# Kernel tuning notes

Hardware: AMD Instinct MI355X
Metric: run time of the kernel (lower is better)

The kernel has to match this reference:

```python
import jax, jax.numpy as jnp
import numpy as np
from jax import lax

B, V, ENC = 64, 2048, 128   # batch, total_voxels, encoder_dim
T = 100                      # max caption length
EMB, DEC, ATT, VOCAB = 256, 512, 256, 29


def setup_inputs() -> dict:
    key = jax.random.key(0)
    ks = jax.random.split(key, 24)
    u = lambda k, shape, s=0.1: jax.random.uniform(k, shape, jnp.float32, -s, s)
    inp = {}
    inp['encoder_output'] = jax.random.normal(ks[0], (B, V, ENC), jnp.float32)
    inp['captions'] = jax.random.randint(ks[1], (B, T), 0, VOCAB)
    # lengths sorted descending (torch loop assumes this); max length == T
    lens = jnp.sort(jax.random.randint(ks[2], (B,), 1, T + 1))[::-1]
    inp['caption_lengths'] = lens.at[0].set(T)
    # parameters (torch Linear: y = x @ W.T + b; kaiming-ish uniform)
    inp['emb_W'] = u(ks[3], (VOCAB, EMB))                       # embed init uniform(-0.1,0.1)
    inp['W_enc'] = u(ks[4], (ATT, ENC), ENC ** -0.5)
    inp['b_enc'] = u(ks[5], (ATT,), ENC ** -0.5)
    inp['W_dec'] = u(ks[6], (ATT, DEC), DEC ** -0.5)
    inp['b_dec'] = u(ks[7], (ATT,), DEC ** -0.5)
    inp['w_full'] = u(ks[8], (ATT,), ATT ** -0.5)               # full_att weight [1,ATT] -> vector
    inp['b_full'] = u(ks[9], (), ATT ** -0.5)
    lstm_in = EMB + ENC
    inp['W_ih'] = u(ks[10], (4 * DEC, lstm_in), DEC ** -0.5)
    inp['b_ih'] = u(ks[11], (4 * DEC,), DEC ** -0.5)
    inp['W_hh'] = u(ks[12], (4 * DEC, DEC), DEC ** -0.5)
    inp['b_hh'] = u(ks[13], (4 * DEC,), DEC ** -0.5)
    inp['W_init_h'] = u(ks[14], (DEC, ENC), ENC ** -0.5)
    inp['b_init_h'] = u(ks[15], (DEC,), ENC ** -0.5)
    inp['W_init_c'] = u(ks[16], (DEC, ENC), ENC ** -0.5)
    inp['b_init_c'] = u(ks[17], (DEC,), ENC ** -0.5)
    inp['W_beta'] = u(ks[18], (ENC, DEC), DEC ** -0.5)
    inp['b_beta'] = u(ks[19], (ENC,), DEC ** -0.5)
    inp['W_final'] = u(ks[20], (VOCAB, DEC))                    # uniform(-0.1,0.1) per init_weights
    inp['b_final'] = jnp.zeros((VOCAB,), jnp.float32)
    return inp


def reference(encoder_output, captions, caption_lengths, emb_W,
              W_enc, b_enc, W_dec, b_dec, w_full, b_full,
              W_ih, b_ih, W_hh, b_hh,
              W_init_h, b_init_h, W_init_c, b_init_c,
              W_beta, b_beta, W_final, b_final):
    # dropout in eval mode (identity) for deterministic reference
    emb = emb_W[captions]                                  # [B,T,EMB]
    enc_att = encoder_output @ W_enc.T + b_enc             # [B,V,ATT] (loop-invariant)
    mean_enc = encoder_output.mean(axis=1)                 # [B,ENC]
    h0 = mean_enc @ W_init_h.T + b_init_h                  # [B,DEC]
    c0 = mean_enc @ W_init_c.T + b_init_c
    lengths = caption_lengths

    def step(carry, xs):
        h, c = carry
        emb_t, t = xs                                      # [B,EMB], scalar
        # additive attention
        dec_att = h @ W_dec.T + b_dec                      # [B,ATT]
        scores = jax.nn.relu(enc_att + dec_att[:, None, :]) @ w_full + b_full  # [B,V]
        alpha = jax.nn.softmax(scores, axis=1)
        awe = jnp.einsum('bv,bve->be', alpha, encoder_output)                   # [B,ENC]
        gate = jax.nn.sigmoid(h @ W_beta.T + b_beta)
        awe = gate * awe
        # LSTMCell (torch gate order: i, f, g, o)
        x = jnp.concatenate([emb_t, awe], axis=1)          # [B,EMB+ENC]
        gates = x @ W_ih.T + b_ih + h @ W_hh.T + b_hh      # [B,4*DEC]
        i, f, g, o = jnp.split(gates, 4, axis=1)
        i, f, o = jax.nn.sigmoid(i), jax.nn.sigmoid(f), jax.nn.sigmoid(o)
        g = jnp.tanh(g)
        c_new = f * c + i * g
        h_new = o * jnp.tanh(c_new)
        pred = h_new @ W_final.T + b_final                 # [B,VOCAB]
        # length-based truncation: only rows with t < length are updated
        m = (t < lengths)[:, None]
        h2 = jnp.where(m, h_new, h)
        c2 = jnp.where(m, c_new, c)
        pred = jnp.where(m, pred, 0.0)
        alpha = jnp.where(m, alpha, 0.0)
        return (h2, c2), (pred, alpha)

    (_, _), (preds, alphas) = lax.scan(
        step, (h0, c0), (emb.transpose(1, 0, 2), jnp.arange(T)))
    predictions = preds.transpose(1, 0, 2)                 # [B,T,VOCAB]
    alphas = alphas.transpose(1, 0, 2)                     # [B,T,V]
    return predictions, alphas, caption_lengths
```

## Files before the change

kernel.cpp:

```cpp
#include <hip/hip_runtime.h>
#include <hip/hip_bf16.h>

#define BB 64
#define VV 2048
#define ENCD 128
#define TT 100
#define EMBD 256
#define DECD 512
#define ATTD 256
#define NVOCAB 29

typedef unsigned int u32;
typedef unsigned short u16;
typedef __attribute__((ext_vector_type(2))) float f2;

__device__ __forceinline__ float sigf(float x) { return 1.0f / (1.0f + __expf(-x)); }
__device__ __forceinline__ u16 to_bf16(float f) {
    u32 u = __float_as_uint(f);
    u += 0x7fffu + ((u >> 16) & 1u);
    return (u16)(u >> 16);
}

#if __has_builtin(__builtin_amdgcn_cvt_pk_fp8_f32) && __has_builtin(__builtin_amdgcn_cvt_pk_f32_fp8)
#define HAVE_FP8_CVT 1
#endif

__device__ __forceinline__ u32 fp8_enc(float f) {
#ifdef HAVE_FP8_CVT
    return (u32)__builtin_amdgcn_cvt_pk_fp8_f32(f, f, 0, false) & 0xffu;
#else
    u32 u = __float_as_uint(f);
    u32 s = (u >> 24) & 0x80u;
    u32 a = u & 0x7fffffffu;
    u32 r = a + 0x7FFFFu + ((a >> 20) & 1u);
    int v = (int)(r >> 20) - (120 << 3);
    if (v < 8) v = 0;
    if (v > 0x7E) v = 0x7E;
    return s | (u32)v;
#endif
}
__device__ __forceinline__ void fp8x4_dec(u32 u, float* o) {
#ifdef HAVE_FP8_CVT
    f2 lo = __builtin_amdgcn_cvt_pk_f32_fp8((int)u, false);
    f2 hi = __builtin_amdgcn_cvt_pk_f32_fp8((int)u, true);
    o[0] = lo[0]; o[1] = lo[1]; o[2] = hi[0]; o[3] = hi[1];
#else
    #pragma unroll
    for (int i = 0; i < 4; i++) {
        u32 byte = (u >> (8 * i)) & 0xffu;
        u32 s = (byte & 0x80u) << 24;
        u32 m = byte & 0x7fu;
        o[i] = m ? __uint_as_float(s | ((m + (120u << 3)) << 20)) : __uint_as_float(s);
    }
#endif
}


__global__ __launch_bounds__(256) void k_transpose(const float* __restrict__ W_dec,
                                                   const float* __restrict__ W_beta,
                                                   const float* __restrict__ W_ih,
                                                   const float* __restrict__ W_enc,
                                                   float* __restrict__ W_decT,
                                                   float* __restrict__ W_betaT,
                                                   float* __restrict__ W2T,
                                                   float* __restrict__ W_encT) {
    int i = blockIdx.x * 256 + threadIdx.x;
    if (i < DECD * ATTD) {
        int l = i / ATTD, a = i % ATTD;
        W_decT[i] = W_dec[a * DECD + l];
    } else if (i < DECD * ATTD + DECD * ENCD) {
        int j = i - DECD * ATTD;
        int l = j / ENCD, e = j % ENCD;
        W_betaT[j] = W_beta[e * DECD + l];
    } else if (i < DECD * ATTD + DECD * ENCD + ENCD * 2048) {
        int j = i - (DECD * ATTD + DECD * ENCD);
        int e = j >> 11, g = j & 2047;
        W2T[j] = W_ih[g * 384 + 256 + e];
    } else if (i < DECD * ATTD + DECD * ENCD + ENCD * 2048 + ENCD * ATTD) {
        int j = i - (DECD * ATTD + DECD * ENCD + ENCD * 2048);
        int k = j / ATTD, a = j % ATTD;
        W_encT[j] = W_enc[a * ENCD + k];
    }
}

__global__ __launch_bounds__(256) void k_mean(const float* __restrict__ enc,
                                              float* __restrict__ mpart) {
    int b = blockIdx.x >> 3, chunk = blockIdx.x & 7;
    int t = threadIdx.x;
    int e = t & 127, h = t >> 7;
    __shared__ float red[256];
    const float* src = enc + ((size_t)b * VV + chunk * 256 + h * 128) * ENCD + e;
    float s = 0.f;
    #pragma unroll 16
    for (int v = 0; v < 128; v++) s += src[(size_t)v * ENCD];
    red[t] = s;
    __syncthreads();
    if (t < 128) mpart[((size_t)b * 8 + chunk) * ENCD + t] = red[t] + red[t + 128];
}

__global__ __launch_bounds__(256) void k_enc_att(const float* __restrict__ enc,
                                                 const float* __restrict__ W_encT,
                                                 const float* __restrict__ b_enc,
                                                 unsigned char* __restrict__ enc_att8,
                                                 u16* __restrict__ enc_bf) {
    __shared__ float tile[64][ENCD + 1];
    int b = blockIdx.y, v0 = blockIdx.x * 64;
    int t = threadIdx.x;
    const float* src = enc + ((size_t)b * VV + v0) * ENCD;
    u16* dstb = enc_bf + ((size_t)b * VV + v0) * ENCD;
    for (int i = t; i < 64 * ENCD; i += 256) {
        float x = src[i];
        tile[i >> 7][i & 127] = x;
        dstb[i] = to_bf16(x);
    }
    __syncthreads();
    int vl = t & 63;
    int ag = __builtin_amdgcn_readfirstlane(t >> 6);
    int qq = v0 >> 9, vin = (v0 & 511) + vl;
    unsigned char* dst8 = enc_att8 + (((size_t)(b * 4 + qq) * 256) << 9) + vin;
    for (int ao = 0; ao < 8; ao++) {
        int a0 = ag * 64 + ao * 8;
        float acc[8];
        #pragma unroll
        for (int j = 0; j < 8; j++) acc[j] = b_enc[a0 + j];
        const float* wT = W_encT + a0;
        #pragma unroll 8
        for (int k = 0; k < ENCD; k++) {
            float x = tile[vl][k];
            #pragma unroll
            for (int j = 0; j < 8; j++) acc[j] = fmaf(x, wT[k * ATTD + j], acc[j]);
        }
        #pragma unroll
        for (int j = 0; j < 8; j++)
            dst8[(size_t)(a0 + j) << 9] = (unsigned char)fp8_enc(acc[j]);
    }
}

__global__ __launch_bounds__(512) void k_init(const float* __restrict__ mpart,
                                              const int* __restrict__ lens,
                                              const int* __restrict__ captions,
                                              const float* __restrict__ emb_W,
                                              const float* __restrict__ W_init_h,
                                              const float* __restrict__ b_init_h,
                                              const float* __restrict__ W_init_c,
                                              const float* __restrict__ b_init_c,
                                              const float* __restrict__ W_decT,
                                              const float* __restrict__ b_dec,
                                              const float* __restrict__ W_betaT,
                                              const float* __restrict__ b_beta,
                                              float* __restrict__ c0,
                                              float* __restrict__ xT,
                                              float* __restrict__ dec_att,
                                              float* __restrict__ gate0,
                                              float* __restrict__ out_len) {
    __shared__ float mean[ENCD];
    __shared__ float h_s[DECD];
    int b = blockIdx.x, t = threadIdx.x;
    if (t < ENCD) {
        const float* mp = mpart + (size_t)b * 8 * ENCD + t;
        float s = mp[0];
        #pragma unroll
        for (int i = 1; i < 8; i++) s += mp[(size_t)i * ENCD];
        mean[t] = s * (1.0f / VV);
    }
    __syncthreads();
    {
        int d = t;
        float hh = b_init_h[d], cc = b_init_c[d];
        for (int k = 0; k < ENCD; k++) {
            hh = fmaf(mean[k], W_init_h[d * ENCD + k], hh);
            cc = fmaf(mean[k], W_init_c[d * ENCD + k], cc);
        }
        c0[b * DECD + d] = cc;
        h_s[d] = hh;
        xT[(384 + d) * BB + b] = hh;
    }
    __syncthreads();
    if (t < ATTD) {
        float s2 = b_dec[t];
        for (int l = 0; l < DECD; l++) s2 = fmaf(h_s[l], W_decT[l * ATTD + t], s2);
        dec_att[b * ATTD + t] = s2;
    } else if (t < ATTD + ENCD) {
        int ee = t - ATTD;
        float s2 = b_beta[ee];
        for (int l = 0; l < DECD; l++) s2 = fmaf(h_s[l], W_betaT[l * ENCD + ee], s2);
        gate0[b * ENCD + ee] = sigf(s2);
    } else {
        int k = t - 384;
        int cap = captions[b * TT + 0];
        xT[k * BB + b] = emb_W[cap * EMBD + k];
        xT[(k + 128) * BB + b] = emb_W[cap * EMBD + k + 128];
    }
    if (t == 0) out_len[b] = (float)lens[b];
}


__global__ __launch_bounds__(256) void k_att(const unsigned char* __restrict__ enc_att8,
                                             const u16* __restrict__ enc_bf,
                                             const float* __restrict__ dec_att,
                                             const float* __restrict__ w_full,
                                             const int* __restrict__ lens,
                                             const float* __restrict__ xT,
                                             const float* __restrict__ W_ih,
                                             const float* __restrict__ W_hh,
                                             const float* __restrict__ b_ih,
                                             const float* __restrict__ b_hh,
                                             u16* __restrict__ escoreT,
                                             float* __restrict__ dpartT,
                                             float* __restrict__ pawe,
                                             float* __restrict__ gates_part, int ts) {
    int blk = blockIdx.x, t = threadIdx.x;
    int lane = t & 63, wv = t >> 6;
    if (blk < 256) {
        int b = blk >> 2, qq = blk & 3;
        if (ts >= lens[b]) return;
        __shared__ float sp[4][512];
        __shared__ float esh[512];
        __shared__ float dred[4];
        __shared__ float redw[4][ENCD];
        {
            const uint2* sp2 = (const uint2*)((const u32*)enc_att8 +
                               (((size_t)(b * 4 + qq)) << 15)) + lane;
            const float* db = dec_att + b * ATTD + wv * 64;
            const float* wf = w_full + wv * 64;
            float acc[8];
            #pragma unroll
            for (int j = 0; j < 8; j++) acc[j] = 0.f;
            #pragma unroll 16
            for (int i = 0; i < 64; i++) {
                uint2 u = sp2[(size_t)(wv * 64 + i) * 64];
                float x[8];
                fp8x4_dec(u.x, x);
                fp8x4_dec(u.y, x + 4);
                float da = db[i], wfv = wf[i];
                #pragma unroll
                for (int j = 0; j < 8; j++)
                    acc[j] = fmaf(fmaxf(x[j] + da, 0.f), wfv, acc[j]);
            }
            #pragma unroll
            for (int j = 0; j < 2; j++)
                *(float4*)&sp[wv][8 * lane + 4 * j] =
                    make_float4(acc[4 * j], acc[4 * j + 1], acc[4 * j + 2], acc[4 * j + 3]);
        }
        __syncthreads();
        float sv[2];
        #pragma unroll
        for (int j = 0; j < 2; j++)
            sv[j] = ((sp[0][2 * t + j] + sp[1][2 * t + j]) + sp[2][2 * t + j]) + sp[3][2 * t + j];
        float e0 = __expf(sv[0]), e1 = __expf(sv[1]);
        u32 pk = (u32)to_bf16(e0) | ((u32)to_bf16(e1) << 16);
        ((u32*)escoreT)[(((size_t)ts * BB + b) * VV + (qq << 9)) / 2 + t] = pk;
        esh[2 * t] = e0; esh[2 * t + 1] = e1;
        float ss = e0 + e1;
        for (int o = 32; o > 0; o >>= 1) ss += __shfl_down(ss, o);
        if (lane == 0) dred[wv] = ss;
        __syncthreads();
        if (t == 0) dpartT[((size_t)ts * BB + b) * 4 + qq] =
                        dred[0] + dred[1] + dred[2] + dred[3];
        const u32* eb = (const u32*)enc_bf + ((size_t)b * VV + (qq << 9)) * (ENCD / 2) + lane;
        float a0 = 0.f, a1 = 0.f;
        #pragma unroll 32
        for (int vv = wv; vv < 512; vv += 4) {
            u32 u = eb[(size_t)vv * 64];
            float sc = esh[vv];
            a0 = fmaf(__uint_as_float(u << 16), sc, a0);
            a1 = fmaf(__uint_as_float(u & 0xffff0000u), sc, a1);
        }
        redw[wv][2 * lane] = a0;
        redw[wv][2 * lane + 1] = a1;
        __syncthreads();
        if (t < ENCD)
            pawe[((size_t)b * 4 + qq) * ENCD + t] =
                redw[0][t] + redw[1][t] + redw[2][t] + redw[3][t];
    } else {
        int idx = blk - 256;
        int kcp = idx >> 6;
        int kc = kcp < 2 ? kcp : kcp + 1;
        int gt = idx & 63;
        int gbase = gt * 32 + wv * 8;
        int gb = __builtin_amdgcn_readfirstlane(gbase);
        int k0 = kc * 128;
        float acc[8];
        #pragma unroll
        for (int j = 0; j < 8; j++)
            acc[j] = (kc == 0) ? (b_ih[gb + j] + b_hh[gb + j]) : 0.f;
        if (kc < 2) {
            #pragma unroll 16
            for (int kk = 0; kk < 128; kk++) {
                float xv = xT[(k0 + kk) * BB + lane];
                #pragma unroll
                for (int j = 0; j < 8; j++)
                    acc[j] = fmaf(xv, W_ih[(gb + j) * 384 + k0 + kk], acc[j]);
            }
        } else {
            const float* Wh = W_hh + (k0 - 384);
            #pragma unroll 16
            for (int kk = 0; kk < 128; kk++) {
                float xv = xT[(k0 + kk) * BB + lane];
                #pragma unroll
                for (int j = 0; j < 8; j++)
                    acc[j] = fmaf(xv, Wh[(gb + j) * DECD + kk], acc[j]);
            }
        }
        float4* o4 = (float4*)(gates_part + ((size_t)kcp * BB + lane) * 2048 + gbase);
        o4[0] = make_float4(acc[0], acc[1], acc[2], acc[3]);
        o4[1] = make_float4(acc[4], acc[5], acc[6], acc[7]);
    }
}

__global__ __launch_bounds__(512) void k_cell(const float* __restrict__ gates_part,
                                              const float* __restrict__ dpartT,
                                              const float* __restrict__ pawe,
                                              const int* __restrict__ lens,
                                              const int* __restrict__ captions,
                                              const float* __restrict__ emb_W,
                                              const float* __restrict__ W2T,
                                              const float* __restrict__ W_final,
                                              const float* __restrict__ b_final,
                                              const float* __restrict__ W_decT,
                                              const float* __restrict__ b_dec,
                                              const float* __restrict__ W_betaT,
                                              const float* __restrict__ b_beta,
                                              float* __restrict__ gate0,
                                              float* __restrict__ gate1,
                                              float* __restrict__ c0,
                                              float* __restrict__ c1,
                                              float* __restrict__ xT,
                                              float* __restrict__ dec_att,
                                              float* __restrict__ preds, int ts) {
    int b = blockIdx.x >> 2, part = blockIdx.x & 3;
    if (ts >= lens[b]) return;
    __shared__ float gawe_s[ENCD];
    __shared__ float h_s[DECD];
    __shared__ float red[512];
    int t = threadIdx.x;
    const float* dp = dpartT + ((size_t)ts * BB + b) * 4;
    float inv = 1.0f / ((dp[0] + dp[1]) + (dp[2] + dp[3]));
    const float* gprev = (ts & 1) ? gate1 : gate0;
    float*       gnext = (ts & 1) ? gate0 : gate1;
    if (t < ENCD) {
        const float* pw = pawe + (size_t)b * 4 * ENCD + t;
        float aw = ((pw[0] + pw[ENCD]) + (pw[2 * ENCD] + pw[3 * ENCD])) * inv;
        gawe_s[t] = gprev[b * ENCD + t] * aw;
    }
    __syncthreads();
    const float* cin  = (ts & 1) ? c1 : c0;
    float*       cout = (ts & 1) ? c0 : c1;
    {
        float gi = 0.f, gf = 0.f, gg = 0.f, go = 0.f;
        #pragma unroll
        for (int sc = 0; sc < 6; sc++) {
            const float* gp = gates_part + ((size_t)sc * BB + b) * 2048;
            gi += gp[t]; gf += gp[512 + t]; gg += gp[1024 + t]; go += gp[1536 + t];
        }
        #pragma unroll 16
        for (int e = 0; e < ENCD; e++) {
            const float* w = W2T + (size_t)e * 2048;
            float ge = gawe_s[e];
            gi = fmaf(w[t], ge, gi);
            gf = fmaf(w[512 + t], ge, gf);
            gg = fmaf(w[1024 + t], ge, gg);
            go = fmaf(w[1536 + t], ge, go);
        }
        gi = sigf(gi); gf = sigf(gf); go = sigf(go); gg = tanhf(gg);
        float cn = fmaf(gf, cin[b * DECD + t], gi * gg);
        float hn = go * tanhf(cn);
        h_s[t] = hn;
        if (part == 0) {
            cout[b * DECD + t] = cn;
            xT[(384 + t) * BB + b] = hn;
        }
    }
    __syncthreads();
    if (part < 2) {
        int a = (t & 127) + part * 128, qq = t >> 7;
        float s = 0.f;
        const float* wd = W_decT + (size_t)qq * 128 * ATTD + a;
        #pragma unroll 16
        for (int l = 0; l < 128; l++) s = fmaf(h_s[qq * 128 + l], wd[(size_t)l * ATTD], s);
        red[t] = s;
        __syncthreads();
        if (t < 128)
            dec_att[b * ATTD + t + part * 128] =
                red[t] + red[t + 128] + red[t + 256] + red[t + 384] + b_dec[t + part * 128];
    } else if (part == 2) {
        int e = t & 127, qq = t >> 7;
        float s = 0.f;
        const float* wb = W_betaT + (size_t)qq * 128 * ENCD + e;
        #pragma unroll 16
        for (int l = 0; l < 128; l++) s = fmaf(h_s[qq * 128 + l], wb[(size_t)l * ENCD], s);
        red[t] = s;
        __syncthreads();
        if (t < 128)
            gnext[b * ENCD + t] = sigf(red[t] + red[t + 128] + red[t + 256] + red[t + 384]
                                       + b_beta[t]);
    } else {
        int lane = t & 63, wv = t >> 6;
        for (int j = wv; j < NVOCAB; j += 8) {
            float s2 = 0.f;
            #pragma unroll
            for (int i = 0; i < 8; i++)
                s2 = fmaf(h_s[lane + 64 * i], W_final[j * DECD + lane + 64 * i], s2);
            for (int o = 32; o > 0; o >>= 1) s2 += __shfl_down(s2, o);
            if (lane == 0) preds[((size_t)b * TT + ts) * NVOCAB + j] = s2 + b_final[j];
        }
        if (t < 256 && ts + 1 < TT) {
            int cap = captions[b * TT + ts + 1];
            xT[t * BB + b] = emb_W[cap * EMBD + t];
        }
    }
}

__global__ __launch_bounds__(256) void k_alphas(const u16* __restrict__ escoreT,
                                                const float* __restrict__ dpartT,
                                                const int* __restrict__ lens,
                                                float* __restrict__ alphas) {
    int ts = blockIdx.x, b = blockIdx.y, t = threadIdx.x;
    if (ts >= lens[b]) return;
    const float* dp = dpartT + ((size_t)ts * BB + b) * 4;
    float inv = 1.0f / ((dp[0] + dp[1]) + (dp[2] + dp[3]));
    const u32* es = (const u32*)escoreT + ((size_t)ts * BB + b) * VV / 2;
    float2* al = (float2*)(alphas + ((size_t)b * TT + ts) * VV);
    #pragma unroll
    for (int i = t; i < VV / 2; i += 256) {
        u32 u = es[i];
        al[i] = make_float2(__uint_as_float(u << 16) * inv,
                            __uint_as_float(u & 0xffff0000u) * inv);
    }
}

extern "C" void kernel_launch(void* const* d_in, const int* in_sizes, int n_in,
                              void* d_out, int out_size, void* d_ws, size_t ws_size,
                              hipStream_t stream) {
    const float* enc      = (const float*)d_in[0];
    const int*   captions = (const int*)d_in[1];
    const int*   lens     = (const int*)d_in[2];
    const float* emb_W    = (const float*)d_in[3];
    const float* W_enc    = (const float*)d_in[4];
    const float* b_enc    = (const float*)d_in[5];
    const float* W_dec    = (const float*)d_in[6];
    const float* b_dec    = (const float*)d_in[7];
    const float* w_full   = (const float*)d_in[8];
    const float* W_ih     = (const float*)d_in[10];
    const float* b_ih     = (const float*)d_in[11];
    const float* W_hh     = (const float*)d_in[12];
    const float* b_hh     = (const float*)d_in[13];
    const float* W_init_h = (const float*)d_in[14];
    const float* b_init_h = (const float*)d_in[15];
    const float* W_init_c = (const float*)d_in[16];
    const float* b_init_c = (const float*)d_in[17];
    const float* W_beta   = (const float*)d_in[18];
    const float* b_beta   = (const float*)d_in[19];
    const float* W_final  = (const float*)d_in[20];
    const float* b_final  = (const float*)d_in[21];

    float* preds   = (float*)d_out;
    float* alphas  = preds + (size_t)BB * TT * NVOCAB;
    float* out_len = alphas + (size_t)BB * TT * VV;

    char* ws = (char*)d_ws;
    size_t off = 0;
    auto alloc = [&](size_t bytes) {
        char* p = ws + off;
        off += (bytes + 255) & ~(size_t)255;
        return p;
    };
    unsigned char* enc_att8 = (unsigned char*)alloc((size_t)BB * ATTD * VV);
    u16*   enc_bf     = (u16*)  alloc((size_t)BB * VV * ENCD * sizeof(u16));
    u16*   escoreT    = (u16*)  alloc((size_t)TT * BB * VV * sizeof(u16));
    float* dpartT     = (float*)alloc((size_t)TT * BB * 4 * sizeof(float));
    float* pawe       = (float*)alloc((size_t)BB * 4 * ENCD * sizeof(float));
    float* dec_att    = (float*)alloc((size_t)BB * ATTD * sizeof(float));
    float* gate0      = (float*)alloc((size_t)BB * ENCD * sizeof(float));
    float* gate1      = (float*)alloc((size_t)BB * ENCD * sizeof(float));
    float* xT         = (float*)alloc((size_t)896 * BB * sizeof(float));
    float* gates_part = (float*)alloc((size_t)6 * BB * 2048 * sizeof(float));
    float* c0         = (float*)alloc((size_t)BB * DECD * sizeof(float));
    float* c1         = (float*)alloc((size_t)BB * DECD * sizeof(float));
    float* W_decT     = (float*)alloc((size_t)DECD * ATTD * sizeof(float));
    float* W_betaT    = (float*)alloc((size_t)DECD * ENCD * sizeof(float));
    float* W2T        = (float*)alloc((size_t)ENCD * 2048 * sizeof(float));
    float* W_encT     = (float*)alloc((size_t)ENCD * ATTD * sizeof(float));
    float* mpart      = (float*)alloc((size_t)BB * 8 * ENCD * sizeof(float));

    hipMemsetAsync(d_out, 0, (size_t)out_size * sizeof(float), stream);

    k_transpose<<<1920, 256, 0, stream>>>(W_dec, W_beta, W_ih, W_enc,
                                          W_decT, W_betaT, W2T, W_encT);
    k_mean<<<BB * 8, 256, 0, stream>>>(enc, mpart);
    k_enc_att<<<dim3(VV / 64, BB), 256, 0, stream>>>(enc, W_encT, b_enc, enc_att8, enc_bf);
    k_init<<<BB, 512, 0, stream>>>(mpart, lens, captions, emb_W, W_init_h, b_init_h,
                                   W_init_c, b_init_c, W_decT, b_dec, W_betaT, b_beta,
                                   c0, xT, dec_att, gate0, out_len);

    for (int t = 0; t < TT; t++) {
        k_att<<<640, 256, 0, stream>>>(enc_att8, enc_bf, dec_att, w_full, lens, xT,
                                       W_ih, W_hh, b_ih, b_hh, escoreT, dpartT, pawe,
                                       gates_part, t);
        k_cell<<<256, 512, 0, stream>>>(gates_part, dpartT, pawe, lens, captions, emb_W,
                                        W2T, W_final, b_final, W_decT, b_dec, W_betaT,
                                        b_beta, gate0, gate1, c0, c1, xT, dec_att,
                                        preds, t);
    }
    k_alphas<<<dim3(TT, BB), 256, 0, stream>>>(escoreT, dpartT, lens, alphas);
}
```

Before: 4.434 ms.

## Split gated-awe LSTM gate contribution into batched kernel reusing W2T across batch

Moves the W_ih·(gate*awe) contribution out of k_cell, where each of 256 blocks streamed the whole 1 MB W2T slice per batch row, into a new 16-block kernel that computes it for all 64 batch rows at once with the gated awe held in shared memory. Each W2T element is now loaded once per step instead of once per batch row, and the result goes into a seventh gates_part slab. The cost is an extra kernel launch per timestep (100 more launches), low parallelism with only 16 blocks, and computation for rows whose length has already ended.

```diff
diff --git a/kernel.cpp b/kernel.cpp
--- a/kernel.cpp
+++ b/kernel.cpp
@@ -308,13 +308,57 @@
     }
 }
 
+__global__ __launch_bounds__(512) void k_kc2(const float* __restrict__ pawe,
+                                             const float* __restrict__ dpartT,
+                                             const float* __restrict__ gate0,
+                                             const float* __restrict__ gate1,
+                                             const float* __restrict__ W2T,
+                                             float* __restrict__ gates_part, int ts) {
+    __shared__ float gawe_s[BB][ENCD];
+    __shared__ float kc2_s[BB][128];
+    int t = threadIdx.x;
+    int go = blockIdx.x * 128;
+    const float* gprev = (ts & 1) ? gate1 : gate0;
+    #pragma unroll
+    for (int i = 0; i < 16; i++) {
+        int idx = t + i * 512;
+        int b = idx >> 7, e = idx & 127;
+        const float* dp = dpartT + ((size_t)ts * BB + b) * 4;
+        float inv = 1.0f / ((dp[0] + dp[1]) + (dp[2] + dp[3]));
+        const float* pw = pawe + (size_t)b * 4 * ENCD + e;
+        float aw = ((pw[0] + pw[ENCD]) + (pw[2 * ENCD] + pw[3 * ENCD])) * inv;
+        gawe_s[b][e] = gprev[b * ENCD + e] * aw;
+    }
+    __syncthreads();
+    {
+        int g = go + (t & 127);
+        int b0 = (t >> 7) * 16;
+        float acc[16];
+        #pragma unroll
+        for (int j = 0; j < 16; j++) acc[j] = 0.f;
+        #pragma unroll 8
+        for (int e = 0; e < ENCD; e++) {
+            float w = W2T[(size_t)e * 2048 + g];
+            #pragma unroll
+            for (int j = 0; j < 16; j++)
+                acc[j] = fmaf(w, gawe_s[b0 + j][e], acc[j]);
+        }
+        #pragma unroll
+        for (int j = 0; j < 16; j++) kc2_s[b0 + j][t & 127] = acc[j];
+    }
+    __syncthreads();
+    #pragma unroll
+    for (int i = 0; i < 16; i++) {
+        int idx = t + i * 512;
+        int b = idx >> 7, gg = idx & 127;
+        gates_part[((size_t)6 * BB + b) * 2048 + go + gg] = kc2_s[b][gg];
+    }
+}
+
 __global__ __launch_bounds__(512) void k_cell(const float* __restrict__ gates_part,
-                                              const float* __restrict__ dpartT,
-                                              const float* __restrict__ pawe,
                                               const int* __restrict__ lens,
                                               const int* __restrict__ captions,
                                               const float* __restrict__ emb_W,
-                                              const float* __restrict__ W2T,
                                               const float* __restrict__ W_final,
                                               const float* __restrict__ b_final,
                                               const float* __restrict__ W_decT,
@@ -330,20 +374,10 @@
                                               float* __restrict__ preds, int ts) {
     int b = blockIdx.x >> 2, part = blockIdx.x & 3;
     if (ts >= lens[b]) return;
-    __shared__ float gawe_s[ENCD];
     __shared__ float h_s[DECD];
     __shared__ float red[512];
     int t = threadIdx.x;
-    const float* dp = dpartT + ((size_t)ts * BB + b) * 4;
-    float inv = 1.0f / ((dp[0] + dp[1]) + (dp[2] + dp[3]));
-    const float* gprev = (ts & 1) ? gate1 : gate0;
-    float*       gnext = (ts & 1) ? gate0 : gate1;
-    if (t < ENCD) {
-        const float* pw = pawe + (size_t)b * 4 * ENCD + t;
-        float aw = ((pw[0] + pw[ENCD]) + (pw[2 * ENCD] + pw[3 * ENCD])) * inv;
-        gawe_s[t] = gprev[b * ENCD + t] * aw;
-    }
-    __syncthreads();
+    float* gnext = (ts & 1) ? gate0 : gate1;
     const float* cin  = (ts & 1) ? c1 : c0;
     float*       cout = (ts & 1) ? c0 : c1;
     {
@@ -353,15 +387,8 @@
             const float* gp = gates_part + ((size_t)sc * BB + b) * 2048;
             gi += gp[t]; gf += gp[512 + t]; gg += gp[1024 + t]; go += gp[1536 + t];
         }
-        #pragma unroll 16
-        for (int e = 0; e < ENCD; e++) {
-            const float* w = W2T + (size_t)e * 2048;
-            float ge = gawe_s[e];
-            gi = fmaf(w[t], ge, gi);
-            gf = fmaf(w[512 + t], ge, gf);
-            gg = fmaf(w[1024 + t], ge, gg);
-            go = fmaf(w[1536 + t], ge, go);
-        }
+        const float* g6 = gates_part + ((size_t)6 * BB + b) * 2048;
+        gi += g6[t]; gf += g6[512 + t]; gg += g6[1024 + t]; go += g6[1536 + t];
         gi = sigf(gi); gf = sigf(gf); go = sigf(go); gg = tanhf(gg);
         float cn = fmaf(gf, cin[b * DECD + t], gi * gg);
         float hn = go * tanhf(cn);
@@ -474,7 +501,7 @@
     float* gate0      = (float*)alloc((size_t)BB * ENCD * sizeof(float));
     float* gate1      = (float*)alloc((size_t)BB * ENCD * sizeof(float));
     float* xT         = (float*)alloc((size_t)896 * BB * sizeof(float));
-    float* gates_part = (float*)alloc((size_t)6 * BB * 2048 * sizeof(float));
+    float* gates_part = (float*)alloc((size_t)7 * BB * 2048 * sizeof(float));
     float* c0         = (float*)alloc((size_t)BB * DECD * sizeof(float));
     float* c1         = (float*)alloc((size_t)BB * DECD * sizeof(float));
     float* W_decT     = (float*)alloc((size_t)DECD * ATTD * sizeof(float));
@@ -497,8 +524,9 @@
         k_att<<<640, 256, 0, stream>>>(enc_att8, enc_bf, dec_att, w_full, lens, xT,
                                        W_ih, W_hh, b_ih, b_hh, escoreT, dpartT, pawe,
                                        gates_part, t);
-        k_cell<<<256, 512, 0, stream>>>(gates_part, dpartT, pawe, lens, captions, emb_W,
-                                        W2T, W_final, b_final, W_decT, b_dec, W_betaT,
+        k_kc2<<<16, 512, 0, stream>>>(pawe, dpartT, gate0, gate1, W2T, gates_part, t);
+        k_cell<<<256, 512, 0, stream>>>(gates_part, lens, captions, emb_W,
+                                        W_final, b_final, W_decT, b_dec, W_betaT,
                                         b_beta, gate0, gate1, c0, c1, xT, dec_att,
                                         preds, t);
     }
```

Result: slower. 7.537 ms (+70.0%).
